# Kernel tuning notes

Hardware: AMD Instinct MI355X
Metric: run time of the kernel (lower is better)

Reference implementation:

```python
import jax, jax.numpy as jnp
import numpy as np

T, B, F = 512, 512, 14
H1, H2 = 32, 64


def setup_inputs() -> dict:
    key = jax.random.key(0)
    ks = jax.random.split(key, 16)
    s1 = 1.0 / np.sqrt(H1)
    s2 = 1.0 / np.sqrt(H2)
    u = lambda k, shape, s: jax.random.uniform(k, shape, jnp.float32, -s, s)
    return {
        "x": jax.random.normal(ks[0], (T, B, F), jnp.float32),
        # LSTM layer 1 (PyTorch gate order i,f,g,o)
        "W_ih1": u(ks[1], (4 * H1, F), s1),
        "W_hh1": u(ks[2], (4 * H1, H1), s1),
        "b_ih1": u(ks[3], (4 * H1,), s1),
        "b_hh1": u(ks[4], (4 * H1,), s1),
        # LSTM layer 2
        "W_ih2": u(ks[5], (4 * H2, H1), s2),
        "W_hh2": u(ks[6], (4 * H2, H2), s2),
        "b_ih2": u(ks[7], (4 * H2,), s2),
        "b_hh2": u(ks[8], (4 * H2,), s2),
        # MLP head
        "W_fc1": u(ks[9], (8, H2), 1.0 / np.sqrt(H2)),
        "b_fc1": u(ks[10], (8,), 1.0 / np.sqrt(H2)),
        "W_fc2": u(ks[11], (8, 8), 1.0 / np.sqrt(8)),
        "b_fc2": u(ks[12], (8,), 1.0 / np.sqrt(8)),
        "W_fc": u(ks[13], (1, 8), 1.0 / np.sqrt(8)),
        "b_fc": u(ks[14], (1,), 1.0 / np.sqrt(8)),
    }


def _gates(g, c):
    # PyTorch LSTM gate order: input, forget, cell(g), output
    i, f, gg, o = jnp.split(g, 4, axis=-1)
    c_new = jax.nn.sigmoid(f) * c + jax.nn.sigmoid(i) * jnp.tanh(gg)
    h_new = jax.nn.sigmoid(o) * jnp.tanh(c_new)
    return h_new, c_new


def reference(x, W_ih1, W_hh1, b_ih1, b_hh1, W_ih2, W_hh2, b_ih2, b_hh2,
              W_fc1, b_fc1, W_fc2, b_fc2, W_fc, b_fc):
    Bv = x.shape[1]
    # Fold the input projection of layer 1 outside the scan (one big GEMM).
    xg = jnp.einsum('tbf,gf->tbg', x, W_ih1) + b_ih1 + b_hh1  # [T,B,4H1]

    def step(carry, xg_t):
        h1, c1, h2 = carry
        h1, c1 = _gates(xg_t + h1 @ W_hh1.T, c1)
        # Layer 2: original code never carries c_t2 -> incoming cell is always 0.
        g2 = h1 @ W_ih2.T + b_ih2 + h2 @ W_hh2.T + b_hh2
        h2, _ = _gates(g2, jnp.zeros((Bv, H2), x.dtype))
        return (h1, c1, h2), None

    init = (jnp.zeros((Bv, H1), x.dtype),
            jnp.zeros((Bv, H1), x.dtype),
            jnp.zeros((Bv, H2), x.dtype))
    (h1, c1, h2), _ = jax.lax.scan(step, init, xg)

    out = jax.nn.relu(h2)
    out = jax.nn.relu(out @ W_fc1.T + b_fc1)
    out = jax.nn.relu(out @ W_fc2.T + b_fc2)
    return out @ W_fc.T + b_fc  # [B,1]
```

## Files before the change

kernel.cpp:

```cpp
#include <hip/hip_runtime.h>
#include <math.h>

#define TT 512
#define BB 512
#define FF 14
#define H1 32
#define H2 64
#define NR 16
#define NBLK (BB / NR)

typedef _Float16 half8   __attribute__((ext_vector_type(8)));
typedef _Float16 half4_t __attribute__((ext_vector_type(4)));
typedef float    float4v __attribute__((ext_vector_type(4)));

typedef __attribute__((address_space(1))) const half4_t g_half4;

#if __has_builtin(__builtin_amdgcn_exp2f)
__device__ __forceinline__ float exp2_(float x) { return __builtin_amdgcn_exp2f(x); }
#else
__device__ __forceinline__ float exp2_(float x) { return exp2f(x); }
#endif
__device__ __forceinline__ float rcpf_(float x) { return __builtin_amdgcn_rcpf(x); }

#define K1L 1.4426950408889634f
#define K2L 2.8853901617779268f

__device__ __forceinline__ float4v mfma16(half8 a, half8 b, float4v c) {
    return __builtin_amdgcn_mfma_f32_16x16x32_f16(a, b, c, 0, 0, 0);
}

__device__ __forceinline__ int bfrag_off(int k, int n) {
    const int slab = k >> 5, k5 = k & 31;
    const int dl = n + 16 * ((k5 >> 3) & 3);
    const int dw = (k5 >> 1) & 3;
    return ((slab * 256 + dl * 4 + dw) << 1) | (k5 & 1);
}

__global__ __launch_bounds__(512)
void xg_precompute(const float* __restrict__ x,
                   const float* __restrict__ Wih1,
                   const float* __restrict__ bih1,
                   const float* __restrict__ bhh1,
                   _Float16* __restrict__ xg)
{
    const int t    = blockIdx.x >> 2;
    const int seg  = blockIdx.x & 3;
    const int l    = threadIdx.x;
    const int lane = l & 63;
    const int w    = l >> 6;
    const int n    = lane & 15;
    const int quad = lane >> 4;
    const int u1   = w * 4 + quad;

    float wr[4][FF];
    float bs[4];
    #pragma unroll
    for (int r = 0; r < 4; ++r) {
        const int row = r * 32 + u1;
        #pragma unroll
        for (int f = 0; f < FF; ++f) wr[r][f] = Wih1[row * FF + f];
        bs[r] = bih1[row] + bhh1[row];
    }

    half4_t* og = (half4_t*)xg + (size_t)t * (NBLK * 512) + l;
    #pragma unroll 2
    for (int bi = 0; bi < 8; ++bi) {
        const int blk = seg * 8 + bi;
        const float* xp = x + ((size_t)t * BB + blk * NR + n) * FF;
        float xv[FF];
        #pragma unroll
        for (int e = 0; e < 7; ++e) {
            const float2 v = *(const float2*)(xp + 2 * e);
            xv[2 * e] = v.x; xv[2 * e + 1] = v.y;
        }
        half4_t o16;
        #pragma unroll
        for (int r = 0; r < 4; ++r) {
            float a = bs[r];
            #pragma unroll
            for (int f = 0; f < FF; ++f) a = fmaf(xv[f], wr[r][f], a);
            o16[r] = (_Float16)a;
        }
        og[(size_t)blk * 512] = o16;
    }
}

#define XGOFF(t_) ((size_t)(t_) * (NBLK * 512))

__global__ __launch_bounds__(512)
__attribute__((amdgpu_waves_per_eu(2, 2)))
void lstm3_v20(
    const _Float16* __restrict__ xg,
    const float* __restrict__ Wih2, const float* __restrict__ Whh1,
    const float* __restrict__ Whh2,
    const float* __restrict__ bih2, const float* __restrict__ bhh2,
    const float* __restrict__ Wfc1, const float* __restrict__ bfc1,
    const float* __restrict__ Wfc2, const float* __restrict__ bfc2,
    const float* __restrict__ Wfc,  const float* __restrict__ bfc,
    float* __restrict__ out)
{
    const int row0 = blockIdx.x * NR;
    const int l    = threadIdx.x;
    const int lane = l & 63;
    const int w    = l >> 6;
    const int n    = lane & 15;
    const int quad = lane >> 4;

    __shared__ __align__(16) unsigned s2f[2][3 * 256];
    __shared__ _Float16 h2plain[NR][H2];
    __shared__ float mlp1[NR][8];
    __shared__ float mlp2[NR][8];

    half8 a2[2][3];
    float4v bias2[2];
    #pragma unroll
    for (int tt = 0; tt < 2; ++tt) {
        const int T = 2 * w + tt;
        const int m = T * 16 + n;
        const int row = (m & 3) * 64 + (m >> 2);
        #pragma unroll
        for (int s = 0; s < 3; ++s) {
            const int k0 = s * 32 + quad * 8;
            half8 a;
            if (k0 < H1) {
                #pragma unroll
                for (int j = 0; j < 8; ++j) a[j] = (_Float16)Wih2[row * H1 + k0 + j];
            } else {
                #pragma unroll
                for (int j = 0; j < 8; ++j) a[j] = (_Float16)Whh2[row * H2 + (k0 - H1) + j];
            }
            a2[tt][s] = a;
        }
        const int u = T * 4 + quad;
        #pragma unroll
        for (int r = 0; r < 4; ++r) {
            const int br = r * 64 + u;
            bias2[tt][r] = bih2[br] + bhh2[br];
        }
    }

    half8 a1h;
    {
        const int m = w * 16 + n;
        const int row = (m & 3) * 32 + (m >> 2);
        #pragma unroll
        for (int j = 0; j < 8; ++j)
            a1h[j] = (_Float16)Whh1[row * H1 + quad * 8 + j];
    }

    const int u1   = w * 4 + quad;
    const int offB = bfrag_off(u1, n);
    int off2[2];
    #pragma unroll
    for (int tt = 0; tt < 2; ++tt)
        off2[tt] = bfrag_off(32 + (2 * w + tt) * 4 + quad, n);

    const g_half4* xgb = (const g_half4*)((const half4_t*)xg + (size_t)blockIdx.x * 512 + l);

    float c1r = 0.0f;

    for (int z = l; z < 2 * 3 * 256; z += 512) ((unsigned*)s2f)[z] = 0u;

    half4_t xg0 = xgb[XGOFF(0)];
    half4_t xgA = xgb[XGOFF(1)];
    half4_t xgB = xgb[XGOFF(2)];
    half4_t xgC = xgb[XGOFF(3)];
    half4_t xgD = xgb[XGOFF(4)];
    __syncthreads();

#define LSTM_STEP(i_, CP_, RP_, XG_) do {                                          \
        const half8 tb0 = *(const half8*)(s2f[RP_] + lane * 4);                    \
        const half8 tb1 = *(const half8*)(s2f[RP_] + 256 + lane * 4);              \
        const half8 tb2 = *(const half8*)(s2f[RP_] + 512 + lane * 4);              \
        const half4_t xh = XG_;             \
        { int tn_ = (i_) + 4; if (tn_ > TT - 1) tn_ = TT - 1;                      \
          XG_ = xgb[XGOFF(tn_)]; }                                                 \
        float4v cin_;                                                              \
        cin_[0] = (float)xh[0]; cin_[1] = (float)xh[1];                            \
        cin_[2] = (float)xh[2]; cin_[3] = (float)xh[3];                            \
        float4v acc1 = mfma16(a1h, tb0, cin_);                                     \
        {   const float Ei = exp2_(-K1L * acc1[0]);                                \
            const float Ef = exp2_(-K1L * acc1[1]);                                \
            const float Eg = exp2_(-K2L * acc1[2]);                                \
            const float Eo = exp2_(-K1L * acc1[3]);                                \
            const float P  = (1.0f + Ei) * (1.0f + Eg);                            \
            const float pf = 1.0f + Ef;                                            \
            const float cn = fmaf(c1r, P, pf * (1.0f - Eg)) * rcpf_(pf * P);       \
            c1r = cn;                                                              \
            const float Ec = exp2_(-K2L * cn);                                     \
            const float hh = (1.0f - Ec) * rcpf_((1.0f + Eo) * (1.0f + Ec));       \
            ((_Float16*)s2f[CP_])[offB] = (_Float16)hh; }                          \
        _Pragma("unroll")                                                          \
        for (int tt = 0; tt < 2; ++tt) {                                           \
            float4v acc = bias2[tt];                                               \
            acc = mfma16(a2[tt][0], tb0, acc);                                     \
            acc = mfma16(a2[tt][1], tb1, acc);                                     \
            acc = mfma16(a2[tt][2], tb2, acc);                                     \
            const float Ei = exp2_(-K1L * acc[0]);                                 \
            const float Eg = exp2_(-K2L * acc[2]);                                 \
            const float Eo = exp2_(-K1L * acc[3]);                                 \
            const float c2 = (1.0f - Eg) * rcpf_((1.0f + Ei) * (1.0f + Eg));       \
            const float Ec = exp2_(-K2L * c2);                                     \
            const float h  = (1.0f - Ec) * rcpf_((1.0f + Eo) * (1.0f + Ec));       \
            ((_Float16*)s2f[CP_])[off2[tt]] = (_Float16)h;                         \
        }                                                                          \
        asm volatile("s_waitcnt lgkmcnt(0)" ::: "memory");                         \
        __builtin_amdgcn_s_barrier();                                              \
        asm volatile("" ::: "memory");                                             \
    } while (0)

    {
        const float gi = (float)xg0[0], gg = (float)xg0[2], go = (float)xg0[3];
        const float Ei = exp2_(-K1L * gi);
        const float Eg = exp2_(-K2L * gg);
        const float Eo = exp2_(-K1L * go);
        const float cn = (1.0f - Eg) * rcpf_((1.0f + Ei) * (1.0f + Eg));
        c1r = cn;
        const float Ec = exp2_(-K2L * cn);
        const float hh = (1.0f - Ec) * rcpf_((1.0f + Eo) * (1.0f + Ec));
        ((_Float16*)s2f[0])[offB] = (_Float16)hh;
        asm volatile("s_waitcnt lgkmcnt(0)" ::: "memory");
        __builtin_amdgcn_s_barrier();
        asm volatile("" ::: "memory");
    }

    #pragma unroll 1
    for (int ii = 0; ii < 127; ++ii) {
        const int i0 = 4 * ii + 1;
        LSTM_STEP(i0,     1, 0, xgA);
        LSTM_STEP(i0 + 1, 0, 1, xgB);
        LSTM_STEP(i0 + 2, 1, 0, xgC);
        LSTM_STEP(i0 + 3, 0, 1, xgD);
    }
    LSTM_STEP(509, 1, 0, xgA);
    LSTM_STEP(510, 0, 1, xgB);
    LSTM_STEP(511, 1, 0, xgC);

    {
        const half8 tb0 = *(const half8*)(s2f[1] + lane * 4);
        const half8 tb1 = *(const half8*)(s2f[1] + 256 + lane * 4);
        const half8 tb2 = *(const half8*)(s2f[1] + 512 + lane * 4);
        #pragma unroll
        for (int tt = 0; tt < 2; ++tt) {
            float4v acc = bias2[tt];
            acc = mfma16(a2[tt][0], tb0, acc);
            acc = mfma16(a2[tt][1], tb1, acc);
            acc = mfma16(a2[tt][2], tb2, acc);
            const float Ei = exp2_(-K1L * acc[0]);
            const float Eg = exp2_(-K2L * acc[2]);
            const float Eo = exp2_(-K1L * acc[3]);
            const float c2 = (1.0f - Eg) * rcpf_((1.0f + Ei) * (1.0f + Eg));
            const float Ec = exp2_(-K2L * c2);
            const float h  = (1.0f - Ec) * rcpf_((1.0f + Eo) * (1.0f + Ec));
            h2plain[n][(2 * w + tt) * 4 + quad] = (_Float16)h;
        }
        __syncthreads();
    }

    if (l < NR * 8) {
        const int rr = l >> 3, j = l & 7;
        float a = bfc1[j];
        #pragma unroll
        for (int k = 0; k < H2; ++k)
            a = fmaf(fmaxf((float)h2plain[rr][k], 0.0f), Wfc1[j * H2 + k], a);
        mlp1[rr][j] = fmaxf(a, 0.0f);
    }
    __syncthreads();
    if (l < NR * 8) {
        const int rr = l >> 3, j = l & 7;
        float a = bfc2[j];
        #pragma unroll
        for (int k = 0; k < 8; ++k) a = fmaf(mlp1[rr][k], Wfc2[j * 8 + k], a);
        mlp2[rr][j] = fmaxf(a, 0.0f);
    }
    __syncthreads();
    if (l < NR) {
        float a = bfc[0];
        #pragma unroll
        for (int k = 0; k < 8; ++k) a = fmaf(mlp2[l][k], Wfc[k], a);
        out[row0 + l] = a;
    }
#undef LSTM_STEP
}

__device__ __forceinline__ float sigmoidf_(float x) { return rcpf_(1.0f + __expf(-x)); }
__device__ __forceinline__ float tanhf_(float x) {
    float e = __expf(-2.0f * fabsf(x));
    float t = (1.0f - e) * rcpf_(1.0f + e);
    return copysignf(t, x);
}

__global__ __launch_bounds__(512)
__attribute__((amdgpu_waves_per_eu(2, 2)))
void lstm3_kernel(
    const float* __restrict__ x,
    const float* __restrict__ Wih1, const float* __restrict__ Whh1,
    const float* __restrict__ bih1, const float* __restrict__ bhh1,
    const float* __restrict__ Wih2, const float* __restrict__ Whh2,
    const float* __restrict__ bih2, const float* __restrict__ bhh2,
    const float* __restrict__ Wfc1, const float* __restrict__ bfc1,
    const float* __restrict__ Wfc2, const float* __restrict__ bfc2,
    const float* __restrict__ Wfc,  const float* __restrict__ bfc,
    float* __restrict__ out)
{
    const int row0 = blockIdx.x * NR;
    const int l    = threadIdx.x;
    const int lane = l & 63;
    const int w    = l >> 6;
    const int n    = lane & 15;
    const int quad = lane >> 4;

    __shared__ __align__(16) unsigned s2f[2][3 * 256];
    __shared__ _Float16 h2plain[NR][H2];
    __shared__ float mlp1[NR][8];
    __shared__ float mlp2[NR][8];

    half8 a2[2][3];
    float4v bias2[2];
    #pragma unroll
    for (int tt = 0; tt < 2; ++tt) {
        const int T = 2 * w + tt;
        const int m = T * 16 + n;
        const int row = (m & 3) * 64 + (m >> 2);
        #pragma unroll
        for (int s = 0; s < 3; ++s) {
            const int k0 = s * 32 + quad * 8;
            half8 a;
            if (k0 < H1) {
                #pragma unroll
                for (int j = 0; j < 8; ++j) a[j] = (_Float16)Wih2[row * H1 + k0 + j];
            } else {
                #pragma unroll
                for (int j = 0; j < 8; ++j) a[j] = (_Float16)Whh2[row * H2 + (k0 - H1) + j];
            }
            a2[tt][s] = a;
        }
        const int u = T * 4 + quad;
        #pragma unroll
        for (int r = 0; r < 4; ++r) {
            const int br = r * 64 + u;
            bias2[tt][r] = bih2[br] + bhh2[br];
        }
    }

    half8 a1x, a1h;
    float4v bias1;
    {
        const int m = w * 16 + n;
        const int row = (m & 3) * 32 + (m >> 2);
        #pragma unroll
        for (int j = 0; j < 8; ++j) {
            const int k = quad * 8 + j;
            a1x[j] = (_Float16)((k < FF) ? Wih1[row * FF + k] : 0.0f);
            a1h[j] = (_Float16)Whh1[row * H1 + k];
        }
        const int u1_ = w * 4 + quad;
        #pragma unroll
        for (int r = 0; r < 4; ++r) {
            const int br = r * 32 + u1_;
            bias1[r] = bih1[br] + bhh1[br];
        }
    }

    const int u1   = w * 4 + quad;
    const int offB = bfrag_off(u1, n);
    int off2[2];
    #pragma unroll
    for (int tt = 0; tt < 2; ++tt)
        off2[tt] = bfrag_off(32 + (2 * w + tt) * 4 + quad, n);

    const int b1q  = quad & 1;
    const int xrow = (row0 + n) * FF;
    const int xo0 = 8 * b1q;
    const int xo1 = 8 * b1q + 2;
    const int xo2 = 8 * b1q + 4;
    const int xo3 = 6 * b1q + 6;

    float c1r = 0.0f;
    float2 xr0[4], xr1[4];

    for (int z = l; z < 2 * 3 * 256; z += 512) ((unsigned*)s2f)[z] = 0u;

    {
        const float* xp = x + xrow;
        xr0[0] = *(const float2*)(xp + xo0);
        xr0[1] = *(const float2*)(xp + xo1);
        xr0[2] = *(const float2*)(xp + xo2);
        xr0[3] = *(const float2*)(xp + xo3);
        const float* xq = x + BB * FF + xrow;
        xr1[0] = *(const float2*)(xq + xo0);
        xr1[1] = *(const float2*)(xq + xo1);
        xr1[2] = *(const float2*)(xq + xo2);
        xr1[3] = *(const float2*)(xq + xo3);
    }
    __syncthreads();

#define LSTM_STEP_F(i_, CP_, RP_, XR_) do {                                        \
        const half8 tb0 = *(const half8*)(s2f[RP_] + lane * 4);                    \
        const half8 tb1 = *(const half8*)(s2f[RP_] + 256 + lane * 4);              \
        const half8 tb2 = *(const half8*)(s2f[RP_] + 512 + lane * 4);              \
        half8 xb;                                                                  \
        xb[0] = (_Float16)XR_[0].x; xb[1] = (_Float16)XR_[0].y;                    \
        xb[2] = (_Float16)XR_[1].x; xb[3] = (_Float16)XR_[1].y;                    \
        xb[4] = (_Float16)XR_[2].x; xb[5] = (_Float16)XR_[2].y;                    \
        xb[6] = (_Float16)XR_[3].x; xb[7] = (_Float16)XR_[3].y;                    \
        { int tn_ = (i_) + 2; if (tn_ > TT - 1) tn_ = TT - 1;                      \
          const float* xp_ = x + tn_ * (BB * FF) + xrow;                           \
          XR_[0] = *(const float2*)(xp_ + xo0);                                    \
          XR_[1] = *(const float2*)(xp_ + xo1);                                    \
          XR_[2] = *(const float2*)(xp_ + xo2);                                    \
          XR_[3] = *(const float2*)(xp_ + xo3); }                                  \
        float4v acc1 = mfma16(a1x, xb, bias1);                                     \
        acc1 = mfma16(a1h, tb0, acc1);                                             \
        const float cn1 = sigmoidf_(acc1[1]) * c1r                                 \
                        + sigmoidf_(acc1[0]) * tanhf_(acc1[2]);                    \
        c1r = cn1;                                                                 \
        ((_Float16*)s2f[CP_])[offB] = (_Float16)(sigmoidf_(acc1[3]) * tanhf_(cn1));\
        _Pragma("unroll")                                                          \
        for (int tt = 0; tt < 2; ++tt) {                                           \
            float4v acc = bias2[tt];                                               \
            acc = mfma16(a2[tt][0], tb0, acc);                                     \
            acc = mfma16(a2[tt][1], tb1, acc);                                     \
            acc = mfma16(a2[tt][2], tb2, acc);                                     \
            const float cn = sigmoidf_(acc[0]) * tanhf_(acc[2]);                   \
            const float h  = sigmoidf_(acc[3]) * tanhf_(cn);                       \
            ((_Float16*)s2f[CP_])[off2[tt]] = (_Float16)h;                         \
        }                                                                          \
        asm volatile("s_waitcnt lgkmcnt(0)" ::: "memory");                         \
        __builtin_amdgcn_s_barrier();                                              \
        asm volatile("" ::: "memory");                                             \
    } while (0)

    {
        half8 xb;
        xb[0] = (_Float16)xr0[0].x; xb[1] = (_Float16)xr0[0].y;
        xb[2] = (_Float16)xr0[1].x; xb[3] = (_Float16)xr0[1].y;
        xb[4] = (_Float16)xr0[2].x; xb[5] = (_Float16)xr0[2].y;
        xb[6] = (_Float16)xr0[3].x; xb[7] = (_Float16)xr0[3].y;
        {   const float* xp_ = x + 2 * (BB * FF) + xrow;
            xr0[0] = *(const float2*)(xp_ + xo0);
            xr0[1] = *(const float2*)(xp_ + xo1);
            xr0[2] = *(const float2*)(xp_ + xo2);
            xr0[3] = *(const float2*)(xp_ + xo3); }
        float4v acc1 = mfma16(a1x, xb, bias1);
        const float cn1 = sigmoidf_(acc1[0]) * tanhf_(acc1[2]);
        c1r = cn1;
        ((_Float16*)s2f[0])[offB] = (_Float16)(sigmoidf_(acc1[3]) * tanhf_(cn1));
        asm volatile("s_waitcnt lgkmcnt(0)" ::: "memory");
        __builtin_amdgcn_s_barrier();
        asm volatile("" ::: "memory");
    }

    #pragma unroll 1
    for (int ii = 0; ii < 255; ++ii) {
        const int i0 = 2 * ii + 1;
        LSTM_STEP_F(i0,     1, 0, xr1);
        LSTM_STEP_F(i0 + 1, 0, 1, xr0);
    }
    LSTM_STEP_F(511, 1, 0, xr1);

    {
        const half8 tb0 = *(const half8*)(s2f[1] + lane * 4);
        const half8 tb1 = *(const half8*)(s2f[1] + 256 + lane * 4);
        const half8 tb2 = *(const half8*)(s2f[1] + 512 + lane * 4);
        #pragma unroll
        for (int tt = 0; tt < 2; ++tt) {
            float4v acc = bias2[tt];
            acc = mfma16(a2[tt][0], tb0, acc);
            acc = mfma16(a2[tt][1], tb1, acc);
            acc = mfma16(a2[tt][2], tb2, acc);
            const float cn = sigmoidf_(acc[0]) * tanhf_(acc[2]);
            const float h  = sigmoidf_(acc[3]) * tanhf_(cn);
            h2plain[n][(2 * w + tt) * 4 + quad] = (_Float16)h;
        }
        __syncthreads();
    }

    if (l < NR * 8) {
        const int rr = l >> 3, j = l & 7;
        float a = bfc1[j];
        #pragma unroll
        for (int k = 0; k < H2; ++k)
            a = fmaf(fmaxf((float)h2plain[rr][k], 0.0f), Wfc1[j * H2 + k], a);
        mlp1[rr][j] = fmaxf(a, 0.0f);
    }
    __syncthreads();
    if (l < NR * 8) {
        const int rr = l >> 3, j = l & 7;
        float a = bfc2[j];
        #pragma unroll
        for (int k = 0; k < 8; ++k) a = fmaf(mlp1[rr][k], Wfc2[j * 8 + k], a);
        mlp2[rr][j] = fmaxf(a, 0.0f);
    }
    __syncthreads();
    if (l < NR) {
        float a = bfc[0];
        #pragma unroll
        for (int k = 0; k < 8; ++k) a = fmaf(mlp2[l][k], Wfc[k], a);
        out[row0 + l] = a;
    }
#undef LSTM_STEP_F
}

extern "C" void kernel_launch(void* const* d_in, const int* in_sizes, int n_in,
                              void* d_out, int out_size, void* d_ws, size_t ws_size,
                              hipStream_t stream) {
    const float* x    = (const float*)d_in[0];
    const float* Wih1 = (const float*)d_in[1];
    const float* Whh1 = (const float*)d_in[2];
    const float* bih1 = (const float*)d_in[3];
    const float* bhh1 = (const float*)d_in[4];
    const float* Wih2 = (const float*)d_in[5];
    const float* Whh2 = (const float*)d_in[6];
    const float* bih2 = (const float*)d_in[7];
    const float* bhh2 = (const float*)d_in[8];
    const float* Wfc1 = (const float*)d_in[9];
    const float* bfc1 = (const float*)d_in[10];
    const float* Wfc2 = (const float*)d_in[11];
    const float* bfc2 = (const float*)d_in[12];
    const float* Wfc  = (const float*)d_in[13];
    const float* bfc  = (const float*)d_in[14];
    float* out = (float*)d_out;

    const size_t xg_bytes = (size_t)TT * BB * (4 * H1) * sizeof(_Float16);
    if (d_ws != nullptr && ws_size >= xg_bytes) {
        _Float16* xg = (_Float16*)d_ws;
        xg_precompute<<<dim3(TT * 4), dim3(512), 0, stream>>>(x, Wih1, bih1, bhh1, xg);
        lstm3_v20<<<dim3(NBLK), dim3(512), 0, stream>>>(
            xg, Wih2, Whh1, Whh2, bih2, bhh2,
            Wfc1, bfc1, Wfc2, bfc2, Wfc, bfc, out);
    } else {
        lstm3_kernel<<<dim3(NBLK), dim3(512), 0, stream>>>(
            x, Wih1, Whh1, bih1, bhh1, Wih2, Whh2, bih2, bhh2,
            Wfc1, bfc1, Wfc2, bfc2, Wfc, bfc, out);
    }
}
```

Before: 360.6 us.

## Halve batch rows per block and merge layer-2 tiles via DPP lane swap

Each block now handles 8 batch rows instead of 16, which doubles the grid to 64 blocks so more compute units run the sequential recurrence. Inside the MFMA tiles only half the columns are useful, so the two layer-2 gate tiles are combined with a DPP row-rotate-by-8 and a lane select. Each lane then evaluates a single set of layer-2 activations instead of two, cutting transcendental work on the serial path. The xg precompute layout and its grid are changed to the 8-row packing, and the fallback kernel is pinned to 16 rows. The trade-off is that half of each MFMA's columns are wasted and a cross-lane DPP move is added to every timestep.

```diff
diff --git a/kernel.cpp b/kernel.cpp
--- a/kernel.cpp
+++ b/kernel.cpp
@@ -6,7 +6,7 @@
 #define FF 14
 #define H1 32
 #define H2 64
-#define NR 16
+#define NR 8
 #define NBLK (BB / NR)
 
 typedef _Float16 half8   __attribute__((ext_vector_type(8)));
@@ -21,6 +21,11 @@
 __device__ __forceinline__ float exp2_(float x) { return exp2f(x); }
 #endif
 __device__ __forceinline__ float rcpf_(float x) { return __builtin_amdgcn_rcpf(x); }
+
+__device__ __forceinline__ float dpp_ror8_(float v) {
+    return __int_as_float(__builtin_amdgcn_update_dpp(
+        0, __float_as_int(v), 0x128 , 0xF, 0xF, true));
+}
 
 #define K1L 1.4426950408889634f
 #define K2L 2.8853901617779268f
@@ -43,8 +48,8 @@
                    const float* __restrict__ bhh1,
                    _Float16* __restrict__ xg)
 {
-    const int t    = blockIdx.x >> 2;
-    const int seg  = blockIdx.x & 3;
+    const int t    = blockIdx.x >> 3;
+    const int seg  = blockIdx.x & 7;
     const int l    = threadIdx.x;
     const int lane = l & 63;
     const int w    = l >> 6;
@@ -62,11 +67,12 @@
         bs[r] = bih1[row] + bhh1[row];
     }
 
-    half4_t* og = (half4_t*)xg + (size_t)t * (NBLK * 512) + l;
+    half4_t* og = (half4_t*)xg + (size_t)t * (NBLK * 256);
     #pragma unroll 2
     for (int bi = 0; bi < 8; ++bi) {
         const int blk = seg * 8 + bi;
-        const float* xp = x + ((size_t)t * BB + blk * NR + n) * FF;
+        const int row = blk * NR + (n & 7);
+        const float* xp = x + ((size_t)t * BB + row) * FF;
         float xv[FF];
         #pragma unroll
         for (int e = 0; e < 7; ++e) {
@@ -81,15 +87,15 @@
             for (int f = 0; f < FF; ++f) a = fmaf(xv[f], wr[r][f], a);
             o16[r] = (_Float16)a;
         }
-        og[(size_t)blk * 512] = o16;
-    }
-}
-
-#define XGOFF(t_) ((size_t)(t_) * (NBLK * 512))
+        if (n < 8) og[blk * 256 + w * 32 + quad * 8 + n] = o16;
+    }
+}
+
+#define XGOFF(t_) ((size_t)(t_) * (NBLK * 256))
 
 __global__ __launch_bounds__(512)
 __attribute__((amdgpu_waves_per_eu(2, 2)))
-void lstm3_v20(
+void lstm3_v21(
     const _Float16* __restrict__ xg,
     const float* __restrict__ Wih2, const float* __restrict__ Whh1,
     const float* __restrict__ Whh2,
@@ -105,6 +111,7 @@
     const int w    = l >> 6;
     const int n    = lane & 15;
     const int quad = lane >> 4;
+    const int hi   = n >> 3;
 
     __shared__ __align__(16) unsigned s2f[2][3 * 256];
     __shared__ _Float16 h2plain[NR][H2];
@@ -148,14 +155,13 @@
             a1h[j] = (_Float16)Whh1[row * H1 + quad * 8 + j];
     }
 
-    const int u1   = w * 4 + quad;
-    const int offB = bfrag_off(u1, n);
-    int off2[2];
-    #pragma unroll
-    for (int tt = 0; tt < 2; ++tt)
-        off2[tt] = bfrag_off(32 + (2 * w + tt) * 4 + quad, n);
-
-    const g_half4* xgb = (const g_half4*)((const half4_t*)xg + (size_t)blockIdx.x * 512 + l);
+    const int u1    = w * 4 + quad;
+    const int offB  = bfrag_off(u1, n);
+    const int u2sel = (2 * w + hi) * 4 + quad;
+    const int off2n = bfrag_off(32 + u2sel, n & 7);
+
+    const g_half4* xgb = (const g_half4*)((const half4_t*)xg
+                        + (size_t)blockIdx.x * 256 + (w * 32 + quad * 8 + (n & 7)));
 
     float c1r = 0.0f;
 
@@ -190,20 +196,27 @@
             const float Ec = exp2_(-K2L * cn);                                     \
             const float hh = (1.0f - Ec) * rcpf_((1.0f + Eo) * (1.0f + Ec));       \
             ((_Float16*)s2f[CP_])[offB] = (_Float16)hh; }                          \
+        float4v p0 = bias2[0];                                                     \
+        p0 = mfma16(a2[0][0], tb0, p0);                                            \
+        p0 = mfma16(a2[0][1], tb1, p0);                                            \
+        p0 = mfma16(a2[0][2], tb2, p0);                                            \
+        float4v p1 = bias2[1];                                                     \
+        p1 = mfma16(a2[1][0], tb0, p1);                                            \
+        p1 = mfma16(a2[1][1], tb1, p1);                                            \
+        p1 = mfma16(a2[1][2], tb2, p1);                                            \
+        float4v ps;                                                                \
         _Pragma("unroll")                                                          \
-        for (int tt = 0; tt < 2; ++tt) {                                           \
-            float4v acc = bias2[tt];                                               \
-            acc = mfma16(a2[tt][0], tb0, acc);                                     \
-            acc = mfma16(a2[tt][1], tb1, acc);                                     \
-            acc = mfma16(a2[tt][2], tb2, acc);                                     \
-            const float Ei = exp2_(-K1L * acc[0]);                                 \
-            const float Eg = exp2_(-K2L * acc[2]);                                 \
-            const float Eo = exp2_(-K1L * acc[3]);                                 \
+        for (int r = 0; r < 4; ++r) {                                              \
+            const float sw = dpp_ror8_(p1[r]);                                     \
+            ps[r] = hi ? sw : p0[r];                                               \
+        }                                                                          \
+        {   const float Ei = exp2_(-K1L * ps[0]);                                  \
+            const float Eg = exp2_(-K2L * ps[2]);                                  \
+            const float Eo = exp2_(-K1L * ps[3]);                                  \
             const float c2 = (1.0f - Eg) * rcpf_((1.0f + Ei) * (1.0f + Eg));       \
             const float Ec = exp2_(-K2L * c2);                                     \
             const float h  = (1.0f - Ec) * rcpf_((1.0f + Eo) * (1.0f + Ec));       \
-            ((_Float16*)s2f[CP_])[off2[tt]] = (_Float16)h;                         \
-        }                                                                          \
+            ((_Float16*)s2f[CP_])[off2n] = (_Float16)h; }                          \
         asm volatile("s_waitcnt lgkmcnt(0)" ::: "memory");                         \
         __builtin_amdgcn_s_barrier();                                              \
         asm volatile("" ::: "memory");                                             \
@@ -240,20 +253,27 @@
         const half8 tb0 = *(const half8*)(s2f[1] + lane * 4);
         const half8 tb1 = *(const half8*)(s2f[1] + 256 + lane * 4);
         const half8 tb2 = *(const half8*)(s2f[1] + 512 + lane * 4);
-        #pragma unroll
-        for (int tt = 0; tt < 2; ++tt) {
-            float4v acc = bias2[tt];
-            acc = mfma16(a2[tt][0], tb0, acc);
-            acc = mfma16(a2[tt][1], tb1, acc);
-            acc = mfma16(a2[tt][2], tb2, acc);
-            const float Ei = exp2_(-K1L * acc[0]);
-            const float Eg = exp2_(-K2L * acc[2]);
-            const float Eo = exp2_(-K1L * acc[3]);
-            const float c2 = (1.0f - Eg) * rcpf_((1.0f + Ei) * (1.0f + Eg));
-            const float Ec = exp2_(-K2L * c2);
-            const float h  = (1.0f - Ec) * rcpf_((1.0f + Eo) * (1.0f + Ec));
-            h2plain[n][(2 * w + tt) * 4 + quad] = (_Float16)h;
-        }
+        float4v p0 = bias2[0];
+        p0 = mfma16(a2[0][0], tb0, p0);
+        p0 = mfma16(a2[0][1], tb1, p0);
+        p0 = mfma16(a2[0][2], tb2, p0);
+        float4v p1 = bias2[1];
+        p1 = mfma16(a2[1][0], tb0, p1);
+        p1 = mfma16(a2[1][1], tb1, p1);
+        p1 = mfma16(a2[1][2], tb2, p1);
+        float4v ps;
+        #pragma unroll
+        for (int r = 0; r < 4; ++r) {
+            const float sw = dpp_ror8_(p1[r]);
+            ps[r] = hi ? sw : p0[r];
+        }
+        const float Ei = exp2_(-K1L * ps[0]);
+        const float Eg = exp2_(-K2L * ps[2]);
+        const float Eo = exp2_(-K1L * ps[3]);
+        const float c2 = (1.0f - Eg) * rcpf_((1.0f + Ei) * (1.0f + Eg));
+        const float Ec = exp2_(-K2L * c2);
+        const float h  = (1.0f - Ec) * rcpf_((1.0f + Eo) * (1.0f + Ec));
+        h2plain[n & 7][u2sel] = (_Float16)h;
         __syncthreads();
     }
 
@@ -303,7 +323,7 @@
     const float* __restrict__ Wfc,  const float* __restrict__ bfc,
     float* __restrict__ out)
 {
-    const int row0 = blockIdx.x * NR;
+    const int row0 = blockIdx.x * 16;
     const int l    = threadIdx.x;
     const int lane = l & 63;
     const int w    = l >> 6;
@@ -311,9 +331,9 @@
     const int quad = lane >> 4;
 
     __shared__ __align__(16) unsigned s2f[2][3 * 256];
-    __shared__ _Float16 h2plain[NR][H2];
-    __shared__ float mlp1[NR][8];
-    __shared__ float mlp2[NR][8];
+    __shared__ _Float16 h2plain[16][H2];
+    __shared__ float mlp1[16][8];
+    __shared__ float mlp2[16][8];
 
     half8 a2[2][3];
     float4v bias2[2];
@@ -476,7 +496,7 @@
         __syncthreads();
     }
 
-    if (l < NR * 8) {
+    if (l < 16 * 8) {
         const int rr = l >> 3, j = l & 7;
         float a = bfc1[j];
         #pragma unroll
@@ -485,7 +505,7 @@
         mlp1[rr][j] = fmaxf(a, 0.0f);
     }
     __syncthreads();
-    if (l < NR * 8) {
+    if (l < 16 * 8) {
         const int rr = l >> 3, j = l & 7;
         float a = bfc2[j];
         #pragma unroll
@@ -493,7 +513,7 @@
         mlp2[rr][j] = fmaxf(a, 0.0f);
     }
     __syncthreads();
-    if (l < NR) {
+    if (l < 16) {
         float a = bfc[0];
         #pragma unroll
         for (int k = 0; k < 8; ++k) a = fmaf(mlp2[l][k], Wfc[k], a);
@@ -522,15 +542,15 @@
     const float* bfc  = (const float*)d_in[14];
     float* out = (float*)d_out;
 
-    const size_t xg_bytes = (size_t)TT * BB * (4 * H1) * sizeof(_Float16);
+    const size_t xg_bytes = (size_t)TT * NBLK * 256 * sizeof(half4_t);
     if (d_ws != nullptr && ws_size >= xg_bytes) {
         _Float16* xg = (_Float16*)d_ws;
-        xg_precompute<<<dim3(TT * 4), dim3(512), 0, stream>>>(x, Wih1, bih1, bhh1, xg);
-        lstm3_v20<<<dim3(NBLK), dim3(512), 0, stream>>>(
+        xg_precompute<<<dim3(TT * 8), dim3(512), 0, stream>>>(x, Wih1, bih1, bhh1, xg);
+        lstm3_v21<<<dim3(NBLK), dim3(512), 0, stream>>>(
             xg, Wih2, Whh1, Whh2, bih2, bhh2,
             Wfc1, bfc1, Wfc2, bfc2, Wfc, bfc, out);
     } else {
-        lstm3_kernel<<<dim3(NBLK), dim3(512), 0, stream>>>(
+        lstm3_kernel<<<dim3(BB / 16), dim3(512), 0, stream>>>(
             x, Wih1, Whh1, bih1, bhh1, Wih2, Whh2, bih2, bhh2,
             Wfc1, bfc1, Wfc2, bfc2, Wfc, bfc, out);
     }
```

After: 356.4 us. About the same (-1.2%).
